# Optimization experiments

Hardware: AMD Instinct MI355X
Metric: run time of the kernel (lower is better)

The kernel has to match this reference:

```python
import jax, jax.numpy as jnp
import numpy as np

B, T, C, H = 4, 2048, 768, 12
D = C // H  # head dim = 64

def setup_inputs() -> dict:
    key = jax.random.key(0)
    k1, k2, k3 = jax.random.split(key, 3)
    x = jax.random.normal(k1, (B, T, C), dtype=jnp.float32)
    W_attn = jax.random.normal(k2, (C, 3 * C), dtype=jnp.float32) * 0.02
    b_attn = jnp.zeros((3 * C,), dtype=jnp.float32)
    W_proj = jax.random.normal(k3, (C, C), dtype=jnp.float32) * 0.02
    b_proj = jnp.zeros((C,), dtype=jnp.float32)
    return {"x": x, "W_attn": W_attn, "b_attn": b_attn, "W_proj": W_proj, "b_proj": b_proj}

def reference(x, W_attn, b_attn, W_proj, b_proj):
    Bx, Tx, Cx = x.shape
    qkv = x @ W_attn + b_attn                      # [B,T,3C]
    q, k, v = jnp.split(qkv, 3, axis=2)
    q = q.reshape(Bx, Tx, H, D).swapaxes(1, 2)     # [B,H,T,D]
    k = k.reshape(Bx, Tx, H, D).swapaxes(1, 2)
    v = v.reshape(Bx, Tx, H, D).swapaxes(1, 2)
    att = jnp.einsum('bhqd,bhkd->bhqk', q, k) / jnp.sqrt(jnp.float32(D))
    mask = jnp.tril(jnp.ones((Tx, Tx), dtype=bool))
    att = jnp.where(mask, att, -jnp.inf)
    att = jax.nn.softmax(att, axis=-1)
    y = jnp.einsum('bhqk,bhkd->bhqd', att, v)      # [B,H,T,D]
    y = y.swapaxes(1, 2).reshape(Bx, Tx, Cx)
    return y @ W_proj + b_proj
```

## Files before the change

### kernel.cpp

```cpp
#include <hip/hip_runtime.h>
#include <hip/hip_bf16.h>

#define BATCH 4
#define TSEQ  2048
#define CDIM  768
#define HNUM  12
#define DHEAD 64
#define NQKV  (3*CDIM)
#define BTOT  (BATCH*TSEQ)
#define BH    (BATCH*HNUM)

typedef unsigned short u16;
typedef __attribute__((ext_vector_type(8))) __bf16 bf16x8;
typedef __attribute__((ext_vector_type(4))) float f32x4;

#define MFMA16(a,b,c) __builtin_amdgcn_mfma_f32_16x16x32_bf16((a),(b),(c),0,0,0)

__device__ __forceinline__ u16 f2b(float f) {
    union { float f; unsigned u; } v; v.f = f;
    unsigned u = v.u;
    unsigned r = (u + 0x7fffu + ((u >> 16) & 1u)) >> 16;
    return (u16)r;
}

__device__ __forceinline__ unsigned cvtpk(float lo, float hi) {
    unsigned r;
    asm("v_cvt_pk_bf16_f32 %0, %1, %2" : "=v"(r) : "v"(lo), "v"(hi));
    return r;
}

__device__ __forceinline__ void gload_lds(const void* g, void* l) {
    __builtin_amdgcn_global_load_lds(
        (const __attribute__((address_space(1))) void*)g,
        (__attribute__((address_space(3))) void*)l, 16, 0, 0);
}

__global__ __launch_bounds__(256) void cast_f32_bf16(
        const float* __restrict__ in, u16* __restrict__ out, int n4) {
    int i = blockIdx.x * blockDim.x + threadIdx.x;
    if (i >= n4) return;
    float4 a = reinterpret_cast<const float4*>(in)[i];
    ushort4 o;
    o.x = f2b(a.x); o.y = f2b(a.y); o.z = f2b(a.z); o.w = f2b(a.w);
    reinterpret_cast<ushort4*>(out)[i] = o;
}

__global__ __launch_bounds__(256) void tcast(
        const float* __restrict__ in, u16* __restrict__ out, int R, int Cc) {
    __shared__ float tile[32][33];
    int c0 = blockIdx.x * 32, r0 = blockIdx.y * 32;
    int tx = threadIdx.x, ty = threadIdx.y;
    #pragma unroll
    for (int i = 0; i < 32; i += 8)
        tile[ty + i][tx] = in[(size_t)(r0 + ty + i) * Cc + c0 + tx];
    __syncthreads();
    #pragma unroll
    for (int i = 0; i < 32; i += 8)
        out[(size_t)(c0 + ty + i) * R + r0 + tx] = f2b(tile[tx][ty + i]);
}

template<int MODE>
__global__ __launch_bounds__(256) void gemm_bt(
        const u16* __restrict__ A, const u16* __restrict__ Bt,
        const float* __restrict__ bias,
        u16* __restrict__ qb, u16* __restrict__ kb, u16* __restrict__ vtb,
        float* __restrict__ outf, int M, int N, int K) {
    __shared__ u16 sA[2][128 * 32];
    __shared__ u16 sB[2][128 * 32];
    const int tid = threadIdx.x;
    const int lane = tid & 63;
    const int w = tid >> 6;
    const int wr = w >> 1, wc = w & 1;
    const int m0 = blockIdx.y * 128, n0 = blockIdx.x * 128;

    f32x4 acc[4][4] = {};

    auto stage = [&](int buf, int kt) {
        #pragma unroll
        for (int i = 0; i < 2; ++i) {
            int chunk = i * 256 + tid;
            int row = chunk >> 2, c8 = chunk & 3;
            gload_lds(A  + (size_t)(m0 + row) * K + kt * 32 + c8 * 8, &sA[buf][chunk * 8]);
            gload_lds(Bt + (size_t)(n0 + row) * K + kt * 32 + c8 * 8, &sB[buf][chunk * 8]);
        }
    };

    const int KT = K / 32;
    stage(0, 0);
    __syncthreads();
    for (int kt = 0; kt < KT; ++kt) {
        if (kt + 1 < KT) stage((kt + 1) & 1, kt + 1);
        const u16* cA = sA[kt & 1];
        const u16* cB = sB[kt & 1];
        bf16x8 af[4], bfr[4];
        #pragma unroll
        for (int m = 0; m < 4; ++m)
            af[m] = *(const bf16x8*)&cA[(wr * 64 + m * 16 + (lane & 15)) * 32 + ((lane >> 4) << 3)];
        #pragma unroll
        for (int n = 0; n < 4; ++n)
            bfr[n] = *(const bf16x8*)&cB[(wc * 64 + n * 16 + (lane & 15)) * 32 + ((lane >> 4) << 3)];
        #pragma unroll
        for (int m = 0; m < 4; ++m)
            #pragma unroll
            for (int n = 0; n < 4; ++n)
                acc[m][n] = MFMA16(af[m], bfr[n], acc[m][n]);
        __syncthreads();
    }

    if (MODE == 0) {
        const int which = n0 / CDIM;
        #pragma unroll
        for (int m = 0; m < 4; ++m) {
            #pragma unroll
            for (int n = 0; n < 4; ++n) {
                const int cg = n0 + wc * 64 + n * 16 + (lane & 15);
                const int c  = cg - which * CDIM;
                const int h  = c >> 6, d = c & 63;
                const float bv = bias[cg];
                const int rg0 = m0 + wr * 64 + m * 16 + ((lane >> 4) << 2);
                const int b = rg0 >> 11, t0 = rg0 & (TSEQ - 1);
                const size_t bh = (size_t)(b * HNUM + h);
                if (which == 2) {
                    ushort4 pv;
                    pv.x = f2b(acc[m][n][0] + bv);
                    pv.y = f2b(acc[m][n][1] + bv);
                    pv.z = f2b(acc[m][n][2] + bv);
                    pv.w = f2b(acc[m][n][3] + bv);
                    *(ushort4*)&vtb[(bh * DHEAD + d) * TSEQ + t0] = pv;
                } else {
                    #pragma unroll
                    for (int j = 0; j < 4; ++j) {
                        const float val = acc[m][n][j] + bv;
                        if (which == 0) qb[(bh * TSEQ + t0 + j) * DHEAD + d] = f2b(val * 0.125f);
                        else            kb[(bh * TSEQ + t0 + j) * DHEAD + d] = f2b(val);
                    }
                }
            }
        }
    } else {
        #pragma unroll
        for (int m = 0; m < 4; ++m) {
            #pragma unroll
            for (int n = 0; n < 4; ++n) {
                const int cg = n0 + wc * 64 + n * 16 + (lane & 15);
                const float bv = bias[cg];
                #pragma unroll
                for (int j = 0; j < 4; ++j) {
                    const int rg = m0 + wr * 64 + m * 16 + ((lane >> 4) << 2) + j;
                    outf[(size_t)rg * CDIM + cg] = acc[m][n][j] + bv;
                }
            }
        }
    }
}

__global__ __launch_bounds__(512, 4) void attn_fwd(
        const u16* __restrict__ qb, const u16* __restrict__ kb,
        const u16* __restrict__ vtb, u16* __restrict__ yb) {
    __shared__ u16 sK[2][64 * 64];
    __shared__ u16 sVt[2][64 * 64];
    const int NQT = TSEQ / 128;
    const int qt = (NQT - 1) - (int)(blockIdx.x / BH);
    const int bh = blockIdx.x % BH;
    const int b = bh / HNUM, h = bh % HNUM;
    const int tid = threadIdx.x, lane = tid & 63, w = tid >> 6;
    const int g = lane >> 4, lq = lane & 15;
    const int q0 = qt * 128;
    const int qlo = q0 + w * 16;
    const u16* qbase = qb  + (size_t)bh * TSEQ * DHEAD;
    const u16* kbase = kb  + (size_t)bh * TSEQ * DHEAD;
    const u16* vbase = vtb + (size_t)bh * DHEAD * TSEQ;

    bf16x8 qf[2];
    #pragma unroll
    for (int ks = 0; ks < 2; ++ks)
        qf[ks] = *(const bf16x8*)&qbase[(size_t)(qlo + lq) * DHEAD + ks * 32 + g * 8];

    f32x4 o[4] = {};
    float mx = -__builtin_inff(), ls = 0.f;

    const int srow = tid >> 3;
    const int lcol = (((tid & 7) << 4) ^ ((srow & 7) << 4)) >> 1;

    auto STAGE = [&](int buf, int kt) {
        const int k0 = kt << 6;
        gload_lds(kbase + (size_t)(k0 + srow) * DHEAD + lcol, &sK[buf][tid * 8]);
        gload_lds(vbase + (size_t)srow * TSEQ + k0 + lcol,    &sVt[buf][tid * 8]);
    };

    const int nk = 2 * qt + 2;
    STAGE(0, 0);
    __syncthreads();
    for (int kt = 0; kt < nk; ++kt) {
        const int k0 = kt << 6;
        if (kt + 1 < nk) STAGE((kt + 1) & 1, kt + 1);
        if (k0 <= qlo + 15) {
            const u16* cK = sK[kt & 1];
            const u16* cV = sVt[kt & 1];
            f32x4 s[4];
            #pragma unroll
            for (int n = 0; n < 4; ++n) {
                s[n] = f32x4{0.f, 0.f, 0.f, 0.f};
                #pragma unroll
                for (int ks = 0; ks < 2; ++ks) {
                    int r = n * 16 + lq;
                    int lb = (r * 128 + (ks * 32 + g * 8) * 2) ^ ((r & 7) << 4);
                    bf16x8 kf = *(const bf16x8*)((const char*)cK + lb);
                    s[n] = MFMA16(kf, qf[ks], s[n]);
                }
            }
            if (k0 + 63 > qlo) {
                const int qa = qlo + lq;
                #pragma unroll
                for (int n = 0; n < 4; ++n)
                    #pragma unroll
                    for (int j = 0; j < 4; ++j)
                        if (k0 + n * 16 + g * 4 + j > qa) s[n][j] = -__builtin_inff();
            }
            float tmax = s[0][0];
            #pragma unroll
            for (int n = 0; n < 4; ++n)
                #pragma unroll
                for (int j = 0; j < 4; ++j) tmax = fmaxf(tmax, s[n][j]);
            tmax = fmaxf(tmax, __shfl_xor(tmax, 16));
            tmax = fmaxf(tmax, __shfl_xor(tmax, 32));
            float mnew = fmaxf(mx, tmax);
            float sc = __expf(mx - mnew);
            mx = mnew;
            float rsum = 0.f;
            #pragma unroll
            for (int n = 0; n < 4; ++n)
                #pragma unroll
                for (int j = 0; j < 4; ++j) {
                    float p = __expf(s[n][j] - mnew);
                    s[n][j] = p;
                    rsum += p;
                }
            rsum += __shfl_xor(rsum, 16);
            rsum += __shfl_xor(rsum, 32);
            ls = ls * sc + rsum;
            #pragma unroll
            for (int j = 0; j < 4; ++j) {
                float scj = __shfl(sc, (lane & 48) | ((g << 2) + j));
                #pragma unroll
                for (int n = 0; n < 4; ++n) o[n][j] *= scj;
            }
            unsigned apk[4], bpk[4];
            #pragma unroll
            for (int n = 0; n < 4; ++n) {
                apk[n] = cvtpk(s[n][0], s[n][1]);
                bpk[n] = cvtpk(s[n][2], s[n][3]);
            }
            const int s0l = lq + ((lane & 16) << 1);
            const bool hi = (lane & 32) != 0;
            #pragma unroll
            for (int ks = 0; ks < 2; ++ks) {
                unsigned A0  = (unsigned)__shfl((int)apk[2 * ks],     s0l);
                unsigned B0  = (unsigned)__shfl((int)bpk[2 * ks],     s0l);
                unsigned A1  = (unsigned)__shfl((int)apk[2 * ks + 1], s0l);
                unsigned B1  = (unsigned)__shfl((int)bpk[2 * ks + 1], s0l);
                unsigned A0h = (unsigned)__shfl((int)apk[2 * ks],     s0l + 16);
                unsigned B0h = (unsigned)__shfl((int)bpk[2 * ks],     s0l + 16);
                unsigned A1h = (unsigned)__shfl((int)apk[2 * ks + 1], s0l + 16);
                unsigned B1h = (unsigned)__shfl((int)bpk[2 * ks + 1], s0l + 16);
                union { unsigned u[4]; bf16x8 v; } pa;
                pa.u[0] = hi ? A1  : A0;
                pa.u[1] = hi ? B1  : B0;
                pa.u[2] = hi ? A1h : A0h;
                pa.u[3] = hi ? B1h : B0h;
                #pragma unroll
                for (int n = 0; n < 4; ++n) {
                    int d = n * 16 + lq;
                    int lb = (d * 128 + (ks * 32 + g * 8) * 2) ^ ((d & 7) << 4);
                    bf16x8 vf = *(const bf16x8*)((const char*)cV + lb);
                    o[n] = MFMA16(pa.v, vf, o[n]);
                }
            }
        }
        __syncthreads();
    }

    #pragma unroll
    for (int j = 0; j < 4; ++j) {
        float lj = __shfl(ls, (lane & 48) | ((g << 2) + j));
        float inv = 1.f / lj;
        const int t = qlo + g * 4 + j;
        #pragma unroll
        for (int n = 0; n < 4; ++n) {
            const int c = h * DHEAD + n * 16 + lq;
            yb[((size_t)b * TSEQ + t) * CDIM + c] = f2b(o[n][j] * inv);
        }
    }
}

extern "C" void kernel_launch(void* const* d_in, const int* in_sizes, int n_in,
                              void* d_out, int out_size, void* d_ws, size_t ws_size,
                              hipStream_t stream) {
    const float* x      = (const float*)d_in[0];
    const float* W_attn = (const float*)d_in[1];
    const float* b_attn = (const float*)d_in[2];
    const float* W_proj = (const float*)d_in[3];
    const float* b_proj = (const float*)d_in[4];
    float* out = (float*)d_out;

    u16* ws = (u16*)d_ws;
    u16* xb     = ws;
    u16* yb     = xb;
    u16* WattnT = xb     + (size_t)BTOT * CDIM;
    u16* WprojT = WattnT + (size_t)NQKV * CDIM;
    u16* qb     = WprojT + (size_t)CDIM * CDIM;
    u16* kb     = qb     + (size_t)BH * TSEQ * DHEAD;
    u16* vtb    = kb     + (size_t)BH * TSEQ * DHEAD;

    int n4 = BTOT * CDIM / 4;
    cast_f32_bf16<<<(n4 + 255) / 256, 256, 0, stream>>>(x, xb, n4);
    tcast<<<dim3(NQKV / 32, CDIM / 32), dim3(32, 8), 0, stream>>>(W_attn, WattnT, CDIM, NQKV);
    tcast<<<dim3(CDIM / 32, CDIM / 32), dim3(32, 8), 0, stream>>>(W_proj, WprojT, CDIM, CDIM);

    gemm_bt<0><<<dim3(NQKV / 128, BTOT / 128), 256, 0, stream>>>(
        xb, WattnT, b_attn, qb, kb, vtb, nullptr, BTOT, NQKV, CDIM);

    attn_fwd<<<dim3((TSEQ / 128) * BH), 512, 0, stream>>>(qb, kb, vtb, yb);

    gemm_bt<1><<<dim3(CDIM / 128, BTOT / 128), 256, 0, stream>>>(
        yb, WprojT, b_proj, nullptr, nullptr, nullptr, out, BTOT, CDIM, CDIM);
}
```

Baseline: 152.4 us.

## Balance causal attention blocks and use exp2 softmax with lazy rescaling

Each attention block now pairs a short 64-row query tile (p) with a long one (31-p) across its two halves of waves, so every block runs a similar number of key tiles and the causal triangle is spread evenly over the grid. The softmax switches to raw v_exp_f32 (base 2), with log2(e) folded into the Q scaling in the QKV epilogue. The running-max rescale of the output and row sum is skipped unless some row's max grows by more than 8 in the log2 domain. s_setprio is raised around the MFMA sections and the row-max reduction becomes a tree. Lazy rescaling lets unnormalized probabilities grow to 2^8, which could slightly affect bf16 precision. Waves in the short-tile half sit idle during the later key tiles.

```diff
diff --git a/kernel.cpp b/kernel.cpp
--- a/kernel.cpp
+++ b/kernel.cpp
@@ -26,6 +26,12 @@
 __device__ __forceinline__ unsigned cvtpk(float lo, float hi) {
     unsigned r;
     asm("v_cvt_pk_bf16_f32 %0, %1, %2" : "=v"(r) : "v"(lo), "v"(hi));
+    return r;
+}
+
+__device__ __forceinline__ float fexp2(float x) {
+    float r;
+    asm("v_exp_f32 %0, %1" : "=v"(r) : "v"(x));
     return r;
 }
 
@@ -131,7 +137,7 @@
                     #pragma unroll
                     for (int j = 0; j < 4; ++j) {
                         const float val = acc[m][n][j] + bv;
-                        if (which == 0) qb[(bh * TSEQ + t0 + j) * DHEAD + d] = f2b(val * 0.125f);
+                        if (which == 0) qb[(bh * TSEQ + t0 + j) * DHEAD + d] = f2b(val * 0.1803368801111243f);
                         else            kb[(bh * TSEQ + t0 + j) * DHEAD + d] = f2b(val);
                     }
                 }
@@ -159,14 +165,13 @@
         const u16* __restrict__ vtb, u16* __restrict__ yb) {
     __shared__ u16 sK[2][64 * 64];
     __shared__ u16 sVt[2][64 * 64];
-    const int NQT = TSEQ / 128;
-    const int qt = (NQT - 1) - (int)(blockIdx.x / BH);
+    const int p  = blockIdx.x / BH;
     const int bh = blockIdx.x % BH;
     const int b = bh / HNUM, h = bh % HNUM;
     const int tid = threadIdx.x, lane = tid & 63, w = tid >> 6;
     const int g = lane >> 4, lq = lane & 15;
-    const int q0 = qt * 128;
-    const int qlo = q0 + w * 16;
+    const int qtile = (w < 4) ? p : (31 - p);
+    const int qlo = qtile * 64 + (w & 3) * 16;
     const u16* qbase = qb  + (size_t)bh * TSEQ * DHEAD;
     const u16* kbase = kb  + (size_t)bh * TSEQ * DHEAD;
     const u16* vbase = vtb + (size_t)bh * DHEAD * TSEQ;
@@ -188,7 +193,7 @@
         gload_lds(vbase + (size_t)srow * TSEQ + k0 + lcol,    &sVt[buf][tid * 8]);
     };
 
-    const int nk = 2 * qt + 2;
+    const int nk = 32 - p;
     STAGE(0, 0);
     __syncthreads();
     for (int kt = 0; kt < nk; ++kt) {
@@ -199,8 +204,10 @@
             const u16* cV = sVt[kt & 1];
             f32x4 s[4];
             #pragma unroll
+            for (int n = 0; n < 4; ++n) s[n] = f32x4{0.f, 0.f, 0.f, 0.f};
+            __builtin_amdgcn_s_setprio(1);
+            #pragma unroll
             for (int n = 0; n < 4; ++n) {
-                s[n] = f32x4{0.f, 0.f, 0.f, 0.f};
                 #pragma unroll
                 for (int ks = 0; ks < 2; ++ks) {
                     int r = n * 16 + lq;
@@ -209,6 +216,7 @@
                     s[n] = MFMA16(kf, qf[ks], s[n]);
                 }
             }
+            __builtin_amdgcn_s_setprio(0);
             if (k0 + 63 > qlo) {
                 const int qa = qlo + lq;
                 #pragma unroll
@@ -217,34 +225,37 @@
                     for (int j = 0; j < 4; ++j)
                         if (k0 + n * 16 + g * 4 + j > qa) s[n][j] = -__builtin_inff();
             }
-            float tmax = s[0][0];
-            #pragma unroll
-            for (int n = 0; n < 4; ++n)
-                #pragma unroll
-                for (int j = 0; j < 4; ++j) tmax = fmaxf(tmax, s[n][j]);
+            float t0 = fmaxf(fmaxf(s[0][0], s[0][1]), fmaxf(s[0][2], s[0][3]));
+            float t1 = fmaxf(fmaxf(s[1][0], s[1][1]), fmaxf(s[1][2], s[1][3]));
+            float t2 = fmaxf(fmaxf(s[2][0], s[2][1]), fmaxf(s[2][2], s[2][3]));
+            float t3 = fmaxf(fmaxf(s[3][0], s[3][1]), fmaxf(s[3][2], s[3][3]));
+            float tmax = fmaxf(fmaxf(t0, t1), fmaxf(t2, t3));
             tmax = fmaxf(tmax, __shfl_xor(tmax, 16));
             tmax = fmaxf(tmax, __shfl_xor(tmax, 32));
-            float mnew = fmaxf(mx, tmax);
-            float sc = __expf(mx - mnew);
-            mx = mnew;
+            if (__any(tmax > mx + 8.0f)) {
+                float mnew = fmaxf(mx, tmax);
+                float sc = fexp2(mx - mnew);
+                mx = mnew;
+                ls *= sc;
+                #pragma unroll
+                for (int j = 0; j < 4; ++j) {
+                    float scj = __shfl(sc, (lane & 48) | ((g << 2) + j));
+                    #pragma unroll
+                    for (int n = 0; n < 4; ++n) o[n][j] *= scj;
+                }
+            }
             float rsum = 0.f;
             #pragma unroll
             for (int n = 0; n < 4; ++n)
                 #pragma unroll
                 for (int j = 0; j < 4; ++j) {
-                    float p = __expf(s[n][j] - mnew);
-                    s[n][j] = p;
-                    rsum += p;
+                    float pv = fexp2(s[n][j] - mx);
+                    s[n][j] = pv;
+                    rsum += pv;
                 }
             rsum += __shfl_xor(rsum, 16);
             rsum += __shfl_xor(rsum, 32);
-            ls = ls * sc + rsum;
-            #pragma unroll
-            for (int j = 0; j < 4; ++j) {
-                float scj = __shfl(sc, (lane & 48) | ((g << 2) + j));
-                #pragma unroll
-                for (int n = 0; n < 4; ++n) o[n][j] *= scj;
-            }
+            ls += rsum;
             unsigned apk[4], bpk[4];
             #pragma unroll
             for (int n = 0; n < 4; ++n) {
@@ -268,6 +279,7 @@
                 pa.u[1] = hi ? B1  : B0;
                 pa.u[2] = hi ? A1h : A0h;
                 pa.u[3] = hi ? B1h : B0h;
+                __builtin_amdgcn_s_setprio(1);
                 #pragma unroll
                 for (int n = 0; n < 4; ++n) {
                     int d = n * 16 + lq;
@@ -275,6 +287,7 @@
                     bf16x8 vf = *(const bf16x8*)((const char*)cV + lb);
                     o[n] = MFMA16(pa.v, vf, o[n]);
                 }
+                __builtin_amdgcn_s_setprio(0);
             }
         }
         __syncthreads();
```

Result: slower. 166.9 us (+9.5%).
